# Kernel optimization log

Hardware: AMD Instinct MI355X
Metric: run time of the kernel (lower is better)

The kernel has to match this reference:

```python
import jax, jax.numpy as jnp
import numpy as np

N_GRAPHS = 500  # number of graphs in the batched graph
BN_EPS = 1e-5


def _bn(x, g, b, m, v):
    # eval-mode BatchNorm1d with running stats
    return (x - m) * jax.lax.rsqrt(v + BN_EPS) * g + b


def setup_inputs() -> dict:
    key = jax.random.key(0)
    ks = jax.random.split(key, 40)
    N, E, Din, H, Dout = 50000, 800000, 64, 64, 64
    inp = {}
    inp["x"] = jax.random.normal(ks[0], (N, Din), jnp.float32)
    inp["src"] = jax.random.randint(ks[1], (E,), 0, N)
    inp["dst"] = jax.random.randint(ks[2], (E,), 0, N)
    inp["graph_ids"] = jnp.sort(jax.random.randint(ks[3], (N,), 0, N_GRAPHS))

    def lin(k, i, o):
        return jax.random.normal(k, (i, o), jnp.float32) / np.sqrt(i).astype(np.float32)

    def bn_params(k):
        k1, k2, k3, k4 = jax.random.split(k, 4)
        g = 1.0 + 0.1 * jax.random.normal(k1, (Dout,), jnp.float32)
        b = 0.1 * jax.random.normal(k2, (Dout,), jnp.float32)
        m = 0.1 * jax.random.normal(k3, (Dout,), jnp.float32)
        v = jax.random.uniform(k4, (Dout,), jnp.float32) + 0.5
        return g, b, m, v

    # GIN layer 0: MLP(in->H, ReLU, H->H, ReLU, BN) + learnable eps
    inp["eps0"] = jnp.zeros((), jnp.float32)
    inp["W0a"] = lin(ks[4], Din, H); inp["bb0a"] = jnp.zeros((H,), jnp.float32)
    inp["W0b"] = lin(ks[5], H, H);   inp["bb0b"] = jnp.zeros((H,), jnp.float32)
    inp["g0i"], inp["be0i"], inp["m0i"], inp["v0i"] = bn_params(ks[6])
    inp["g0"], inp["be0"], inp["m0"], inp["v0"] = bn_params(ks[7])
    # GIN layer 1 (last): MLP(H->out, ReLU, BN) + learnable eps
    inp["eps1"] = jnp.zeros((), jnp.float32)
    inp["W1a"] = lin(ks[8], H, Dout); inp["bb1a"] = jnp.zeros((Dout,), jnp.float32)
    inp["g1i"], inp["be1i"], inp["m1i"], inp["v1i"] = bn_params(ks[9])
    inp["g1"], inp["be1"], inp["m1"], inp["v1"] = bn_params(ks[10])
    # readout MLP out->out->out
    inp["Wr1"] = lin(ks[11], Dout, Dout); inp["br1"] = jnp.zeros((Dout,), jnp.float32)
    inp["Wr2"] = lin(ks[12], Dout, Dout); inp["br2"] = jnp.zeros((Dout,), jnp.float32)
    return inp


def reference(x, src, dst, graph_ids, eps0, W0a, bb0a, W0b, bb0b,
              g0i, be0i, m0i, v0i, g0, be0, m0, v0,
              eps1, W1a, bb1a, g1i, be1i, m1i, v1i, g1, be1, m1, v1,
              Wr1, br1, Wr2, br2):
    N = x.shape[0]
    # ---- GIN layer 0: (1+eps)*h + sum_{neighbors} h, then MLP ----
    agg = jax.ops.segment_sum(x[src], dst, num_segments=N)  # [N, Din]
    h = (1.0 + eps0) * x + agg
    h = jax.nn.relu(h @ W0a + bb0a)
    h = jax.nn.relu(h @ W0b + bb0b)
    h = _bn(h, g0i, be0i, m0i, v0i)
    h = jax.nn.relu(_bn(h, g0, be0, m0, v0))  # outer BN + ReLU (dropout: eval mode = identity)
    # ---- GIN layer 1 ----
    agg = jax.ops.segment_sum(h[src], dst, num_segments=N)
    h = (1.0 + eps1) * h + agg
    h = jax.nn.relu(h @ W1a + bb1a)
    h = _bn(h, g1i, be1i, m1i, v1i)
    h = jax.nn.relu(_bn(h, g1, be1, m1, v1))
    # ---- mean_nodes readout per graph ----
    sums = jax.ops.segment_sum(h, graph_ids, num_segments=N_GRAPHS)  # [G, Dout]
    counts = jax.ops.segment_sum(jnp.ones((N,), h.dtype), graph_ids, num_segments=N_GRAPHS)
    hg = sums / jnp.maximum(counts, 1.0)[:, None]
    out = jax.nn.relu(hg @ Wr1 + br1) @ Wr2 + br2  # [G, Dout]
    return (out, h)
```

## Files before the change

### kernel.cpp

```cpp
#include <hip/hip_runtime.h>


#define EPB 2048
#define PER 32
#define MAXB 512
#define NBP 512

typedef __attribute__((ext_vector_type(8))) short short8;
typedef __attribute__((ext_vector_type(4))) float f32x4;

__device__ __forceinline__ unsigned bf16pack(float a, float b) {
    unsigned ua = __float_as_uint(a);
    unsigned ub = __float_as_uint(b);
    ua = (ua + 0x7FFFu + ((ua >> 16) & 1u)) >> 16;
    ub = (ub + 0x7FFFu + ((ub >> 16) & 1u)) & 0xFFFF0000u;
    return ua | ub;
}
__device__ __forceinline__ unsigned short bf16r(float a) {
    unsigned u = __float_as_uint(a);
    return (unsigned short)((u + 0x7FFFu + ((u >> 16) & 1u)) >> 16);
}
__device__ __forceinline__ float bf16lo(unsigned w) { return __uint_as_float(w << 16); }
__device__ __forceinline__ float bf16hi(unsigned w) { return __uint_as_float(w & 0xFFFF0000u); }

__global__ __launch_bounds__(256) void cast_scatter(
    uint4* __restrict__ xb4, const float4* __restrict__ x4, int nq,
    unsigned* __restrict__ ebuf, int* __restrict__ cnts,
    const int* __restrict__ src, const int* __restrict__ dst,
    int E, int NB, int CAPB) {
    __shared__ int h[MAXB];
    const int t = threadIdx.x;
    const int b = blockIdx.x;
    const int nblk = gridDim.x;

    for (int i = b * 256 + t; i < nq; i += nblk * 256) {
        float4 a = x4[2 * i], c = x4[2 * i + 1];
        uint4 o;
        o.x = bf16pack(a.x, a.y); o.y = bf16pack(a.z, a.w);
        o.z = bf16pack(c.x, c.y); o.w = bf16pack(c.z, c.w);
        xb4[i] = o;
    }

    for (int i = t; i < MAXB; i += 256) h[i] = 0;
    __syncthreads();

    const int base = b * EPB;
#pragma unroll
    for (int i = 0; i < 8; ++i) {
        int e = base + i * 256 + t;
        if (e < E) {
            int s = src[e];
            int d = dst[e];
            int k = d >> 7;
            int p = atomicAdd(&h[k], 1);
            if (p < PER)
                ebuf[(size_t)k * CAPB + b * PER + p] =
                    ((unsigned)s << 16) | (unsigned)d;
        }
    }
    __syncthreads();
    for (int i = t; i < NB; i += 256) cnts[(size_t)b * NBP + i] = min(h[i], PER);
}

__global__ __launch_bounds__(256) void bucket_fill2(
    unsigned* __restrict__ ebuf, const int* __restrict__ cnts,
    int* __restrict__ rstart, int* __restrict__ rend,
    float* __restrict__ hg, int hgn,
    int N, int EB, int NB, int CAPB) {
    __shared__ int tbase[256];
    __shared__ unsigned pairLDS[4608];
    __shared__ unsigned colLDS[4608];
    __shared__ int deg[128], off[128], cur[128];
    const int bb = blockIdx.x;
    const int t = threadIdx.x;
    const int nb0 = bb << 7;
    const int CPT = (EB + 255) / 256;

    for (int i = bb * 256 + t; i < hgn; i += NB * 256) hg[i] = 0.f;

    int myc[8];
    int s = 0;
#pragma unroll 4
    for (int k = 0; k < CPT; ++k) {
        int c = t * CPT + k;
        int v = (c < EB) ? cnts[(size_t)c * NBP + bb] : 0;
        myc[k] = v;
        s += v;
    }
    tbase[t] = s;
    __syncthreads();
    for (int o = 1; o < 256; o <<= 1) {
        int u = (t >= o) ? tbase[t - o] : 0;
        __syncthreads();
        tbase[t] += u;
        __syncthreads();
    }
    const int m = tbase[255];
    int wbase = (t > 0) ? tbase[t - 1] : 0;

#pragma unroll 4
    for (int k = 0; k < CPT; ++k) {
        int c = t * CPT + k;
        int cnt = myc[k];
        for (int j = 0; j < cnt; ++j)
            pairLDS[wbase + j] = ebuf[(size_t)bb * CAPB + c * PER + j];
        wbase += cnt;
    }

    if (t < 128) deg[t] = 0;
    __syncthreads();

    for (int k = t; k < m; k += 256)
        atomicAdd(&deg[(int)(pairLDS[k] & 0xFFFFu) - nb0], 1);
    __syncthreads();
    if (t < 128) off[t] = deg[t];
    __syncthreads();
    for (int s2 = 1; s2 < 128; s2 <<= 1) {
        int u = 0;
        if (t < 128 && t >= s2) u = off[t - s2];
        __syncthreads();
        if (t < 128) off[t] += u;
        __syncthreads();
    }
    if (t < 128) {
        int excl = off[t] - deg[t];
        cur[t] = excl;
        int node = nb0 + t;
        if (node < N) {
            rstart[node] = bb * CAPB + excl;
            rend[node] = bb * CAPB + excl + deg[t];
        }
    }
    __syncthreads();
    for (int k = t; k < m; k += 256) {
        unsigned v = pairLDS[k];
        int dl = (int)(v & 0xFFFFu) - nb0;
        int p = atomicAdd(&cur[dl], 1);
        colLDS[p] = v >> 16;
    }
    __syncthreads();
    for (int k = t; k < m; k += 256) ebuf[(size_t)bb * CAPB + k] = colLDS[k];
}

__global__ __launch_bounds__(256) void aggregate_bf16(
    unsigned* __restrict__ outb, const unsigned* __restrict__ inb,
    const int* __restrict__ rstart, const int* __restrict__ rend,
    const unsigned* __restrict__ col, const float* __restrict__ eps, int N) {
    const int n = blockIdx.x * 4 + (threadIdx.x >> 6);
    if (n >= N) return;
    const int lane = threadIdx.x & 63;
    const int q = lane & 7;
    const int jj = lane >> 3;
    const int lo = rstart[n];
    const int hi = rend[n];
    const uint4* in4 = reinterpret_cast<const uint4*>(inb);

    float a[8];
#pragma unroll
    for (int k = 0; k < 8; ++k) a[k] = 0.f;

    int j = lo;
#pragma unroll 2
    for (; j + 8 <= hi; j += 8) {
        unsigned c = col[j + jj];
        uint4 v = in4[(size_t)c * 8 + q];
        a[0] += bf16lo(v.x); a[1] += bf16hi(v.x);
        a[2] += bf16lo(v.y); a[3] += bf16hi(v.y);
        a[4] += bf16lo(v.z); a[5] += bf16hi(v.z);
        a[6] += bf16lo(v.w); a[7] += bf16hi(v.w);
    }
    if (j + jj < hi) {
        unsigned c = col[j + jj];
        uint4 v = in4[(size_t)c * 8 + q];
        a[0] += bf16lo(v.x); a[1] += bf16hi(v.x);
        a[2] += bf16lo(v.y); a[3] += bf16hi(v.y);
        a[4] += bf16lo(v.z); a[5] += bf16hi(v.z);
        a[6] += bf16lo(v.w); a[7] += bf16hi(v.w);
    }

#pragma unroll
    for (int k = 0; k < 8; ++k) {
        a[k] += __shfl_xor(a[k], 8);
        a[k] += __shfl_xor(a[k], 16);
        a[k] += __shfl_xor(a[k], 32);
    }

    if (jj == 0) {
        float s = 1.0f + eps[0];
        uint4 o = in4[(size_t)n * 8 + q];
        a[0] = fmaf(s, bf16lo(o.x), a[0]); a[1] = fmaf(s, bf16hi(o.x), a[1]);
        a[2] = fmaf(s, bf16lo(o.y), a[2]); a[3] = fmaf(s, bf16hi(o.y), a[3]);
        a[4] = fmaf(s, bf16lo(o.z), a[4]); a[5] = fmaf(s, bf16hi(o.z), a[5]);
        a[6] = fmaf(s, bf16lo(o.w), a[6]); a[7] = fmaf(s, bf16hi(o.w), a[7]);
        uint4 w;
        w.x = bf16pack(a[0], a[1]); w.y = bf16pack(a[2], a[3]);
        w.z = bf16pack(a[4], a[5]); w.w = bf16pack(a[6], a[7]);
        reinterpret_cast<uint4*>(outb)[(size_t)n * 8 + q] = w;
    }
}

template <bool TWO, bool OUTB>
__global__ __launch_bounds__(256) void mlp_mfma(
    const unsigned* __restrict__ inb, unsigned* __restrict__ outb,
    float* __restrict__ outf, int N,
    const float* __restrict__ Wa, const float* __restrict__ ba,
    const float* __restrict__ Wb, const float* __restrict__ bb,
    const float* __restrict__ gi, const float* __restrict__ bei,
    const float* __restrict__ mi, const float* __restrict__ vi,
    const float* __restrict__ go, const float* __restrict__ beo,
    const float* __restrict__ mo, const float* __restrict__ vo,
    const int* __restrict__ gid, float* __restrict__ hg) {
    constexpr int PB = 72;
    __shared__ __align__(16) unsigned short XY[64 * PB];
    __shared__ __align__(16) unsigned short W1t[64 * PB];
    __shared__ __align__(16) unsigned short W2t[TWO ? 64 * PB : 8];
    __shared__ float Yf[TWO ? 1 : 64 * 68];
    __shared__ int gidl[TWO ? 1 : 64];

    const int t = threadIdx.x;
    const int row0 = blockIdx.x * 64;
    const int lane = t & 63;
    const int w = t >> 6;
    const int cl = lane & 15;
    const int kg = lane >> 4;

    {
        const uint4* in4 = reinterpret_cast<const uint4*>(inb);
        for (int cc = t; cc < 512; cc += 256) {
            int r = cc >> 3, ch = cc & 7;
            int grow = row0 + r;
            uint4 v = make_uint4(0u, 0u, 0u, 0u);
            if (grow < N) v = in4[(size_t)grow * 8 + ch];
            *reinterpret_cast<uint4*>(&XY[r * PB + ch * 8]) = v;
        }
    }
    for (int p = t; p < 1024; p += 256) {
        int k = p >> 4, c4 = (p & 15) * 4;
        float4 v = *reinterpret_cast<const float4*>(&Wa[k * 64 + c4]);
        W1t[(c4 + 0) * PB + k] = bf16r(v.x);
        W1t[(c4 + 1) * PB + k] = bf16r(v.y);
        W1t[(c4 + 2) * PB + k] = bf16r(v.z);
        W1t[(c4 + 3) * PB + k] = bf16r(v.w);
        if (TWO) {
            float4 u = *reinterpret_cast<const float4*>(&Wb[k * 64 + c4]);
            W2t[(c4 + 0) * PB + k] = bf16r(u.x);
            W2t[(c4 + 1) * PB + k] = bf16r(u.y);
            W2t[(c4 + 2) * PB + k] = bf16r(u.z);
            W2t[(c4 + 3) * PB + k] = bf16r(u.w);
        }
    }
    if (!TWO && t < 64) gidl[t] = (row0 + t < N) ? gid[row0 + t] : -1;
    __syncthreads();

    f32x4 acc[4];
#pragma unroll
    for (int n = 0; n < 4; ++n) acc[n] = (f32x4){0.f, 0.f, 0.f, 0.f};
    const int arow = w * 16 + cl;
#pragma unroll
    for (int kk = 0; kk < 64; kk += 32) {
        short8 af = *reinterpret_cast<const short8*>(&XY[arow * PB + kk + kg * 8]);
#pragma unroll
        for (int n = 0; n < 4; ++n) {
            short8 bf = *reinterpret_cast<const short8*>(
                &W1t[(n * 16 + cl) * PB + kk + kg * 8]);
            acc[n] = __builtin_amdgcn_mfma_f32_16x16x32_bf16(af, bf, acc[n], 0, 0, 0);
        }
    }

    const int rowb = w * 16 + kg * 4;

    if (TWO) {
        __syncthreads();
#pragma unroll
        for (int n = 0; n < 4; ++n) {
            int c = n * 16 + cl;
            float bias = ba[c];
#pragma unroll
            for (int r = 0; r < 4; ++r)
                XY[(rowb + r) * PB + c] = bf16r(fmaxf(acc[n][r] + bias, 0.f));
        }
        __syncthreads();
#pragma unroll
        for (int n = 0; n < 4; ++n) acc[n] = (f32x4){0.f, 0.f, 0.f, 0.f};
#pragma unroll
        for (int kk = 0; kk < 64; kk += 32) {
            short8 af = *reinterpret_cast<const short8*>(&XY[arow * PB + kk + kg * 8]);
#pragma unroll
            for (int n = 0; n < 4; ++n) {
                short8 bf = *reinterpret_cast<const short8*>(
                    &W2t[(n * 16 + cl) * PB + kk + kg * 8]);
                acc[n] = __builtin_amdgcn_mfma_f32_16x16x32_bf16(af, bf, acc[n], 0, 0, 0);
            }
        }
    }

    const float* bias2 = TWO ? bb : ba;
#pragma unroll
    for (int n = 0; n < 4; ++n) {
        int c = n * 16 + cl;
        float si = gi[c] * rsqrtf(vi[c] + 1e-5f);
        float ti = bei[c] - mi[c] * si;
        float so = go[c] * rsqrtf(vo[c] + 1e-5f);
        float to = beo[c] - mo[c] * so;
        float scv = si * so;
        float shv = ti * so + to;
        float bias = bias2[c];
#pragma unroll
        for (int r = 0; r < 4; ++r) {
            int grow = row0 + rowb + r;
            float y = 0.f;
            if (grow < N) {
                float u = fmaxf(acc[n][r] + bias, 0.f);
                y = fmaxf(u * scv + shv, 0.f);
                if (OUTB) {
                    reinterpret_cast<unsigned short*>(outb)[(size_t)grow * 64 + c] =
                        bf16r(y);
                } else {
                    outf[(size_t)grow * 64 + c] = y;
                }
            }
            if (!TWO) Yf[(rowb + r) * 68 + c] = y;
        }
    }

    if (!TWO) {
        __syncthreads();
        if (t < 64) {
            const int c = t;
            float run = 0.f;
            int cg = -2;
            for (int r = 0; r < 64; ++r) {
                int rg = gidl[r];
                if (rg != cg) {
                    if (cg >= 0) atomicAdd(&hg[(size_t)cg * 64 + c], run);
                    run = 0.f;
                    cg = rg;
                }
                if (rg >= 0) run += Yf[r * 68 + c];
            }
            if (cg >= 0) atomicAdd(&hg[(size_t)cg * 64 + c], run);
        }
    }
}

__device__ __forceinline__ int lbound(const int* __restrict__ a, int n, int v) {
    int lo = 0, hi = n;
    while (lo < hi) {
        int mid = (lo + hi) >> 1;
        if (a[mid] < v) lo = mid + 1;
        else hi = mid;
    }
    return lo;
}

__global__ __launch_bounds__(64) void readout_small(
    const float* __restrict__ hg, const int* __restrict__ gid, int N,
    const float* __restrict__ W1, const float* __restrict__ b1,
    const float* __restrict__ W2, const float* __restrict__ b2,
    float* __restrict__ out) {
    __shared__ float hgl[64];
    __shared__ float t1[64];
    const int g = blockIdx.x;
    const int c = threadIdx.x;

    const int lo = lbound(gid, N, g);
    const int hi = lbound(gid, N, g + 1);
    hgl[c] = hg[(size_t)g * 64 + c] / fmaxf((float)(hi - lo), 1.0f);
    __syncthreads();

    float a1 = b1[c];
#pragma unroll 8
    for (int k = 0; k < 64; ++k) a1 = fmaf(hgl[k], W1[k * 64 + c], a1);
    t1[c] = fmaxf(a1, 0.f);
    __syncthreads();

    float a2 = b2[c];
#pragma unroll 8
    for (int k = 0; k < 64; ++k) a2 = fmaf(t1[k], W2[k * 64 + c], a2);
    out[(size_t)g * 64 + c] = a2;
}

extern "C" void kernel_launch(void* const* d_in, const int* in_sizes, int n_in,
                              void* d_out, int out_size, void* d_ws, size_t ws_size,
                              hipStream_t stream) {
    const float* x    = (const float*)d_in[0];
    const int*   src  = (const int*)d_in[1];
    const int*   dst  = (const int*)d_in[2];
    const int*   gid  = (const int*)d_in[3];
    const float* eps0 = (const float*)d_in[4];
    const float* W0a  = (const float*)d_in[5];
    const float* bb0a = (const float*)d_in[6];
    const float* W0b  = (const float*)d_in[7];
    const float* bb0b = (const float*)d_in[8];
    const float* g0i  = (const float*)d_in[9];
    const float* be0i = (const float*)d_in[10];
    const float* m0i  = (const float*)d_in[11];
    const float* v0i  = (const float*)d_in[12];
    const float* g0   = (const float*)d_in[13];
    const float* be0  = (const float*)d_in[14];
    const float* m0   = (const float*)d_in[15];
    const float* v0   = (const float*)d_in[16];
    const float* eps1 = (const float*)d_in[17];
    const float* W1a  = (const float*)d_in[18];
    const float* bb1a = (const float*)d_in[19];
    const float* g1i  = (const float*)d_in[20];
    const float* be1i = (const float*)d_in[21];
    const float* m1i  = (const float*)d_in[22];
    const float* v1i  = (const float*)d_in[23];
    const float* g1   = (const float*)d_in[24];
    const float* be1  = (const float*)d_in[25];
    const float* m1   = (const float*)d_in[26];
    const float* v1   = (const float*)d_in[27];
    const float* Wr1  = (const float*)d_in[28];
    const float* br1  = (const float*)d_in[29];
    const float* Wr2  = (const float*)d_in[30];
    const float* br2  = (const float*)d_in[31];

    const int N = in_sizes[0] / 64;
    const int E = in_sizes[1];
    const int G = out_size / 64 - N;
    const int NB = (N + 127) >> 7;
    const int EB = (E + EPB - 1) / EPB;
    const int CAPB = EB * PER;

    char* ws = (char*)d_ws;
    unsigned* xb     = (unsigned*)ws;      ws += (size_t)N * 32 * 4;
    unsigned* Ab     = (unsigned*)ws;      ws += (size_t)N * 32 * 4;
    unsigned* Z0b    = (unsigned*)ws;      ws += (size_t)N * 32 * 4;
    unsigned* Bb     = (unsigned*)ws;      ws += (size_t)N * 32 * 4;
    int*      rstart = (int*)ws;           ws += ((size_t)N + 8) * 4;
    int*      rend   = (int*)ws;           ws += ((size_t)N + 8) * 4;
    int*      cnts   = (int*)ws;           ws += (size_t)EB * NBP * 4;
    unsigned* ebuf   = (unsigned*)ws;      ws += (size_t)NB * CAPB * 4;
    float*    hg     = (float*)ws;

    float* OUT = (float*)d_out;
    float* H   = OUT + (size_t)G * 64;

    const int NQ = N * 8;

    cast_scatter<<<EB, 256, 0, stream>>>(
        (uint4*)xb, (const float4*)x, NQ, ebuf, cnts, src, dst, E, NB, CAPB);
    bucket_fill2<<<NB, 256, 0, stream>>>(ebuf, cnts, rstart, rend, hg, G * 64,
                                         N, EB, NB, CAPB);

    aggregate_bf16<<<(N + 3) / 4, 256, 0, stream>>>(Ab, xb, rstart, rend, ebuf, eps0, N);
    mlp_mfma<true, true><<<(N + 63) / 64, 256, 0, stream>>>(
        Ab, Z0b, nullptr, N, W0a, bb0a, W0b, bb0b,
        g0i, be0i, m0i, v0i, g0, be0, m0, v0, nullptr, nullptr);

    aggregate_bf16<<<(N + 3) / 4, 256, 0, stream>>>(Bb, Z0b, rstart, rend, ebuf, eps1, N);
    mlp_mfma<false, false><<<(N + 63) / 64, 256, 0, stream>>>(
        Bb, nullptr, H, N, W1a, bb1a, nullptr, nullptr,
        g1i, be1i, m1i, v1i, g1, be1, m1, v1, gid, hg);

    readout_small<<<G, 64, 0, stream>>>(hg, gid, N, Wr1, br1, Wr2, br2, OUT);
}
```

Measured before the change: 111.5 us.

## Fuse neighbor aggregation into MLP kernel per GIN layer

Merges the separate aggregate and MLP kernels into one gin_layer kernel. Each 512-thread block aggregates 32 nodes straight into LDS, then runs the MFMA MLP, with each wave computing one 16x16 output tile. This removes the intermediate bf16 aggregate buffers and their global write/read round trip, plus two launches. The cost is that the weight transpose is now redone over more, smaller blocks, and each wave aggregates 4 nodes serially before a block-wide barrier.

```diff
diff --git a/kernel.cpp b/kernel.cpp
--- a/kernel.cpp
+++ b/kernel.cpp
@@ -142,67 +142,12 @@
     for (int k = t; k < m; k += 256) ebuf[(size_t)bb * CAPB + k] = colLDS[k];
 }
 
-__global__ __launch_bounds__(256) void aggregate_bf16(
-    unsigned* __restrict__ outb, const unsigned* __restrict__ inb,
+template <bool TWO, bool OUTB>
+__global__ __launch_bounds__(512, 8) void gin_layer(
+    const unsigned* __restrict__ inb, unsigned* __restrict__ outb,
+    float* __restrict__ outf,
     const int* __restrict__ rstart, const int* __restrict__ rend,
-    const unsigned* __restrict__ col, const float* __restrict__ eps, int N) {
-    const int n = blockIdx.x * 4 + (threadIdx.x >> 6);
-    if (n >= N) return;
-    const int lane = threadIdx.x & 63;
-    const int q = lane & 7;
-    const int jj = lane >> 3;
-    const int lo = rstart[n];
-    const int hi = rend[n];
-    const uint4* in4 = reinterpret_cast<const uint4*>(inb);
-
-    float a[8];
-#pragma unroll
-    for (int k = 0; k < 8; ++k) a[k] = 0.f;
-
-    int j = lo;
-#pragma unroll 2
-    for (; j + 8 <= hi; j += 8) {
-        unsigned c = col[j + jj];
-        uint4 v = in4[(size_t)c * 8 + q];
-        a[0] += bf16lo(v.x); a[1] += bf16hi(v.x);
-        a[2] += bf16lo(v.y); a[3] += bf16hi(v.y);
-        a[4] += bf16lo(v.z); a[5] += bf16hi(v.z);
-        a[6] += bf16lo(v.w); a[7] += bf16hi(v.w);
-    }
-    if (j + jj < hi) {
-        unsigned c = col[j + jj];
-        uint4 v = in4[(size_t)c * 8 + q];
-        a[0] += bf16lo(v.x); a[1] += bf16hi(v.x);
-        a[2] += bf16lo(v.y); a[3] += bf16hi(v.y);
-        a[4] += bf16lo(v.z); a[5] += bf16hi(v.z);
-        a[6] += bf16lo(v.w); a[7] += bf16hi(v.w);
-    }
-
-#pragma unroll
-    for (int k = 0; k < 8; ++k) {
-        a[k] += __shfl_xor(a[k], 8);
-        a[k] += __shfl_xor(a[k], 16);
-        a[k] += __shfl_xor(a[k], 32);
-    }
-
-    if (jj == 0) {
-        float s = 1.0f + eps[0];
-        uint4 o = in4[(size_t)n * 8 + q];
-        a[0] = fmaf(s, bf16lo(o.x), a[0]); a[1] = fmaf(s, bf16hi(o.x), a[1]);
-        a[2] = fmaf(s, bf16lo(o.y), a[2]); a[3] = fmaf(s, bf16hi(o.y), a[3]);
-        a[4] = fmaf(s, bf16lo(o.z), a[4]); a[5] = fmaf(s, bf16hi(o.z), a[5]);
-        a[6] = fmaf(s, bf16lo(o.w), a[6]); a[7] = fmaf(s, bf16hi(o.w), a[7]);
-        uint4 w;
-        w.x = bf16pack(a[0], a[1]); w.y = bf16pack(a[2], a[3]);
-        w.z = bf16pack(a[4], a[5]); w.w = bf16pack(a[6], a[7]);
-        reinterpret_cast<uint4*>(outb)[(size_t)n * 8 + q] = w;
-    }
-}
-
-template <bool TWO, bool OUTB>
-__global__ __launch_bounds__(256) void mlp_mfma(
-    const unsigned* __restrict__ inb, unsigned* __restrict__ outb,
-    float* __restrict__ outf, int N,
+    const unsigned* __restrict__ col, const float* __restrict__ eps, int N,
     const float* __restrict__ Wa, const float* __restrict__ ba,
     const float* __restrict__ Wb, const float* __restrict__ bb,
     const float* __restrict__ gi, const float* __restrict__ bei,
@@ -211,30 +156,18 @@
     const float* __restrict__ mo, const float* __restrict__ vo,
     const int* __restrict__ gid, float* __restrict__ hg) {
     constexpr int PB = 72;
-    __shared__ __align__(16) unsigned short XY[64 * PB];
+    __shared__ __align__(16) unsigned short XY[32 * PB];
     __shared__ __align__(16) unsigned short W1t[64 * PB];
     __shared__ __align__(16) unsigned short W2t[TWO ? 64 * PB : 8];
-    __shared__ float Yf[TWO ? 1 : 64 * 68];
-    __shared__ int gidl[TWO ? 1 : 64];
+    __shared__ float Yf[TWO ? 1 : 32 * 68];
+    __shared__ int gidl[TWO ? 1 : 32];
 
     const int t = threadIdx.x;
-    const int row0 = blockIdx.x * 64;
+    const int row0 = blockIdx.x * 32;
     const int lane = t & 63;
     const int w = t >> 6;
-    const int cl = lane & 15;
-    const int kg = lane >> 4;
-
-    {
-        const uint4* in4 = reinterpret_cast<const uint4*>(inb);
-        for (int cc = t; cc < 512; cc += 256) {
-            int r = cc >> 3, ch = cc & 7;
-            int grow = row0 + r;
-            uint4 v = make_uint4(0u, 0u, 0u, 0u);
-            if (grow < N) v = in4[(size_t)grow * 8 + ch];
-            *reinterpret_cast<uint4*>(&XY[r * PB + ch * 8]) = v;
-        }
-    }
-    for (int p = t; p < 1024; p += 256) {
+
+    for (int p = t; p < 1024; p += 512) {
         int k = p >> 4, c4 = (p & 15) * 4;
         float4 v = *reinterpret_cast<const float4*>(&Wa[k * 64 + c4]);
         W1t[(c4 + 0) * PB + k] = bf16r(v.x);
@@ -249,55 +182,101 @@
             W2t[(c4 + 3) * PB + k] = bf16r(u.w);
         }
     }
-    if (!TWO && t < 64) gidl[t] = (row0 + t < N) ? gid[row0 + t] : -1;
-    __syncthreads();
-
-    f32x4 acc[4];
-#pragma unroll
-    for (int n = 0; n < 4; ++n) acc[n] = (f32x4){0.f, 0.f, 0.f, 0.f};
-    const int arow = w * 16 + cl;
+    if (!TWO && t < 32) gidl[t] = (row0 + t < N) ? gid[row0 + t] : -1;
+
+    {
+        const int q = lane & 7;
+        const int jj = lane >> 3;
+        const uint4* in4 = reinterpret_cast<const uint4*>(inb);
+        const float s = 1.0f + eps[0];
+        for (int it = 0; it < 4; ++it) {
+            const int r = w * 4 + it;
+            const int n = row0 + r;
+            float a[8];
+#pragma unroll
+            for (int k2 = 0; k2 < 8; ++k2) a[k2] = 0.f;
+            if (n < N) {
+                const int lo = rstart[n];
+                const int hi = rend[n];
+                int j = lo;
+#pragma unroll 2
+                for (; j + 8 <= hi; j += 8) {
+                    unsigned c = col[j + jj];
+                    uint4 v = in4[(size_t)c * 8 + q];
+                    a[0] += bf16lo(v.x); a[1] += bf16hi(v.x);
+                    a[2] += bf16lo(v.y); a[3] += bf16hi(v.y);
+                    a[4] += bf16lo(v.z); a[5] += bf16hi(v.z);
+                    a[6] += bf16lo(v.w); a[7] += bf16hi(v.w);
+                }
+                if (j + jj < hi) {
+                    unsigned c = col[j + jj];
+                    uint4 v = in4[(size_t)c * 8 + q];
+                    a[0] += bf16lo(v.x); a[1] += bf16hi(v.x);
+                    a[2] += bf16lo(v.y); a[3] += bf16hi(v.y);
+                    a[4] += bf16lo(v.z); a[5] += bf16hi(v.z);
+                    a[6] += bf16lo(v.w); a[7] += bf16hi(v.w);
+                }
+            }
+#pragma unroll
+            for (int k2 = 0; k2 < 8; ++k2) {
+                a[k2] += __shfl_xor(a[k2], 8);
+                a[k2] += __shfl_xor(a[k2], 16);
+                a[k2] += __shfl_xor(a[k2], 32);
+            }
+            if (jj == 0) {
+                if (n < N) {
+                    uint4 o = in4[(size_t)n * 8 + q];
+                    a[0] = fmaf(s, bf16lo(o.x), a[0]); a[1] = fmaf(s, bf16hi(o.x), a[1]);
+                    a[2] = fmaf(s, bf16lo(o.y), a[2]); a[3] = fmaf(s, bf16hi(o.y), a[3]);
+                    a[4] = fmaf(s, bf16lo(o.z), a[4]); a[5] = fmaf(s, bf16hi(o.z), a[5]);
+                    a[6] = fmaf(s, bf16lo(o.w), a[6]); a[7] = fmaf(s, bf16hi(o.w), a[7]);
+                }
+                uint4 wv;
+                wv.x = bf16pack(a[0], a[1]); wv.y = bf16pack(a[2], a[3]);
+                wv.z = bf16pack(a[4], a[5]); wv.w = bf16pack(a[6], a[7]);
+                *reinterpret_cast<uint4*>(&XY[r * PB + q * 8]) = wv;
+            }
+        }
+    }
+    __syncthreads();
+
+    const int cl = lane & 15;
+    const int kg = lane >> 4;
+    const int tr = w >> 2;
+    const int tc = w & 3;
+    const int arow = tr * 16 + cl;
+    const int bcol = tc * 16 + cl;
+    const int rowb = tr * 16 + kg * 4;
+    const int c = tc * 16 + cl;
+
+    f32x4 acc = (f32x4){0.f, 0.f, 0.f, 0.f};
 #pragma unroll
     for (int kk = 0; kk < 64; kk += 32) {
         short8 af = *reinterpret_cast<const short8*>(&XY[arow * PB + kk + kg * 8]);
-#pragma unroll
-        for (int n = 0; n < 4; ++n) {
-            short8 bf = *reinterpret_cast<const short8*>(
-                &W1t[(n * 16 + cl) * PB + kk + kg * 8]);
-            acc[n] = __builtin_amdgcn_mfma_f32_16x16x32_bf16(af, bf, acc[n], 0, 0, 0);
-        }
-    }
-
-    const int rowb = w * 16 + kg * 4;
+        short8 bf = *reinterpret_cast<const short8*>(&W1t[bcol * PB + kk + kg * 8]);
+        acc = __builtin_amdgcn_mfma_f32_16x16x32_bf16(af, bf, acc, 0, 0, 0);
+    }
 
     if (TWO) {
         __syncthreads();
-#pragma unroll
-        for (int n = 0; n < 4; ++n) {
-            int c = n * 16 + cl;
+        {
             float bias = ba[c];
 #pragma unroll
             for (int r = 0; r < 4; ++r)
-                XY[(rowb + r) * PB + c] = bf16r(fmaxf(acc[n][r] + bias, 0.f));
-        }
-        __syncthreads();
-#pragma unroll
-        for (int n = 0; n < 4; ++n) acc[n] = (f32x4){0.f, 0.f, 0.f, 0.f};
+                XY[(rowb + r) * PB + c] = bf16r(fmaxf(acc[r] + bias, 0.f));
+        }
+        __syncthreads();
+        acc = (f32x4){0.f, 0.f, 0.f, 0.f};
 #pragma unroll
         for (int kk = 0; kk < 64; kk += 32) {
             short8 af = *reinterpret_cast<const short8*>(&XY[arow * PB + kk + kg * 8]);
-#pragma unroll
-            for (int n = 0; n < 4; ++n) {
-                short8 bf = *reinterpret_cast<const short8*>(
-                    &W2t[(n * 16 + cl) * PB + kk + kg * 8]);
-                acc[n] = __builtin_amdgcn_mfma_f32_16x16x32_bf16(af, bf, acc[n], 0, 0, 0);
-            }
-        }
-    }
-
-    const float* bias2 = TWO ? bb : ba;
-#pragma unroll
-    for (int n = 0; n < 4; ++n) {
-        int c = n * 16 + cl;
+            short8 bf = *reinterpret_cast<const short8*>(&W2t[bcol * PB + kk + kg * 8]);
+            acc = __builtin_amdgcn_mfma_f32_16x16x32_bf16(af, bf, acc, 0, 0, 0);
+        }
+    }
+
+    {
+        const float* bias2 = TWO ? bb : ba;
         float si = gi[c] * rsqrtf(vi[c] + 1e-5f);
         float ti = bei[c] - mi[c] * si;
         float so = go[c] * rsqrtf(vo[c] + 1e-5f);
@@ -310,7 +289,7 @@
             int grow = row0 + rowb + r;
             float y = 0.f;
             if (grow < N) {
-                float u = fmaxf(acc[n][r] + bias, 0.f);
+                float u = fmaxf(acc[r] + bias, 0.f);
                 y = fmaxf(u * scv + shv, 0.f);
                 if (OUTB) {
                     reinterpret_cast<unsigned short*>(outb)[(size_t)grow * 64 + c] =
@@ -326,19 +305,19 @@
     if (!TWO) {
         __syncthreads();
         if (t < 64) {
-            const int c = t;
+            const int cc = t;
             float run = 0.f;
             int cg = -2;
-            for (int r = 0; r < 64; ++r) {
+            for (int r = 0; r < 32; ++r) {
                 int rg = gidl[r];
                 if (rg != cg) {
-                    if (cg >= 0) atomicAdd(&hg[(size_t)cg * 64 + c], run);
+                    if (cg >= 0) atomicAdd(&hg[(size_t)cg * 64 + cc], run);
                     run = 0.f;
                     cg = rg;
                 }
-                if (rg >= 0) run += Yf[r * 68 + c];
+                if (rg >= 0) run += Yf[r * 68 + cc];
             }
-            if (cg >= 0) atomicAdd(&hg[(size_t)cg * 64 + c], run);
+            if (cg >= 0) atomicAdd(&hg[(size_t)cg * 64 + cc], run);
         }
     }
 }
@@ -425,9 +404,7 @@
 
     char* ws = (char*)d_ws;
     unsigned* xb     = (unsigned*)ws;      ws += (size_t)N * 32 * 4;
-    unsigned* Ab     = (unsigned*)ws;      ws += (size_t)N * 32 * 4;
     unsigned* Z0b    = (unsigned*)ws;      ws += (size_t)N * 32 * 4;
-    unsigned* Bb     = (unsigned*)ws;      ws += (size_t)N * 32 * 4;
     int*      rstart = (int*)ws;           ws += ((size_t)N + 8) * 4;
     int*      rend   = (int*)ws;           ws += ((size_t)N + 8) * 4;
     int*      cnts   = (int*)ws;           ws += (size_t)EB * NBP * 4;
@@ -438,21 +415,22 @@
     float* H   = OUT + (size_t)G * 64;
 
     const int NQ = N * 8;
+    const int NGB = (N + 31) / 32;
 
     cast_scatter<<<EB, 256, 0, stream>>>(
         (uint4*)xb, (const float4*)x, NQ, ebuf, cnts, src, dst, E, NB, CAPB);
     bucket_fill2<<<NB, 256, 0, stream>>>(ebuf, cnts, rstart, rend, hg, G * 64,
                                          N, EB, NB, CAPB);
 
-    aggregate_bf16<<<(N + 3) / 4, 256, 0, stream>>>(Ab, xb, rstart, rend, ebuf, eps0, N);
-    mlp_mfma<true, true><<<(N + 63) / 64, 256, 0, stream>>>(
-        Ab, Z0b, nullptr, N, W0a, bb0a, W0b, bb0b,
-        g0i, be0i, m0i, v0i, g0, be0, m0, v0, nullptr, nullptr);
-
-    aggregate_bf16<<<(N + 3) / 4, 256, 0, stream>>>(Bb, Z0b, rstart, rend, ebuf, eps1, N);
-    mlp_mfma<false, false><<<(N + 63) / 64, 256, 0, stream>>>(
-        Bb, nullptr, H, N, W1a, bb1a, nullptr, nullptr,
-        g1i, be1i, m1i, v1i, g1, be1, m1, v1, gid, hg);
+    gin_layer<true, true><<<NGB, 512, 0, stream>>>(
+        xb, Z0b, nullptr, rstart, rend, ebuf, eps0, N,
+        W0a, bb0a, W0b, bb0b, g0i, be0i, m0i, v0i, g0, be0, m0, v0,
+        nullptr, nullptr);
+
+    gin_layer<false, false><<<NGB, 512, 0, stream>>>(
+        Z0b, nullptr, H, rstart, rend, ebuf, eps1, N,
+        W1a, bb1a, nullptr, nullptr, g1i, be1i, m1i, v1i, g1, be1, m1, v1,
+        gid, hg);
 
     readout_small<<<G, 64, 0, stream>>>(hg, gid, N, Wr1, br1, Wr2, br2, OUT);
 }
```

After: 104.3 us. 1.07x faster.
